# Optimization experiments

Hardware: AMD Instinct MI355X
Metric: run time of the kernel (lower is better)

The kernel has to match this reference:

```python
import jax, jax.numpy as jnp
import numpy as np

EARTH_RADIUS = 6371.0
TAU = 75.0
EPS = 1e-9


def setup_inputs() -> dict:
    key = jax.random.key(0)
    k1, k2, k3 = jax.random.split(key, 3)
    B, C = 512, 32768
    pred_logits = jax.random.normal(k1, (B, C), dtype=jnp.float32)
    # lat in [-90, 90], lon in [-180, 180]
    u_true = jax.random.uniform(k2, (B, 2), dtype=jnp.float32)
    latlon = u_true * jnp.array([180.0, 360.0], jnp.float32) - jnp.array([90.0, 180.0], jnp.float32)
    u_geo = jax.random.uniform(k3, (C, 2), dtype=jnp.float32)
    geocell_coords = u_geo * jnp.array([180.0, 360.0], jnp.float32) - jnp.array([90.0, 180.0], jnp.float32)
    return {"pred_logits": pred_logits, "latlon": latlon, "geocell_coords": geocell_coords}


def _haversine_matrix(latlon, geocell_coords):
    # latlon: [B,2] degrees, geocell_coords: [C,2] degrees -> [B,C] km
    t = jnp.deg2rad(latlon)          # [B,2]
    g = jnp.deg2rad(geocell_coords)  # [C,2]
    lat1 = t[:, 0:1]                 # [B,1]
    lon1 = t[:, 1:2]
    lat2 = g[None, :, 0]             # [1,C]
    lon2 = g[None, :, 1]
    dlat = lat2 - lat1               # [B,C]
    dlon = lon2 - lon1
    a = jnp.sin(dlat * 0.5) ** 2 + jnp.cos(lat1) * jnp.cos(lat2) * jnp.sin(dlon * 0.5) ** 2
    return 2.0 * EARTH_RADIUS * jnp.arcsin(jnp.sqrt(a))


def reference(pred_logits, latlon, geocell_coords):
    dist = _haversine_matrix(latlon, geocell_coords)          # [B,C]
    target = jnp.exp(-dist / TAU)                              # [B,C]
    target = target / jnp.sum(target, axis=1, keepdims=True)
    pred_probs = jax.nn.softmax(pred_logits, axis=1)
    loss = jnp.mean(jnp.sum(-target * jnp.log(pred_probs + EPS), axis=1))
    return loss
```

## Files before the change

kernel.cpp:

```cpp
#include <hip/hip_runtime.h>
#include <math.h>

#define PI_F 3.14159265358979323846f

__global__ void geo_precompute(const float* __restrict__ geo,
                               float4* __restrict__ tab, int C,
                               float* __restrict__ out) {
    int c = blockIdx.x * blockDim.x + threadIdx.x;
    if (c == 0) out[0] = 0.0f;
    if (c >= C) return;
    float lat = geo[2 * c + 0] * (PI_F / 180.0f);
    float lon = geo[2 * c + 1] * (PI_F / 180.0f);
    float sla, cla, slo, clo;
    __sincosf(lat, &sla, &cla);
    __sincosf(lon, &slo, &clo);
    tab[c] = make_float4(cla * clo, cla * slo, sla, 0.0f);
}

__device__ __forceinline__ void pair_accum(float l, float4 g,
                                           float v1x, float v1y, float v1z,
                                           float& Z, float& S0, float& S1) {
    float dot = fmaf(g.x, v1x, fmaf(g.y, v1y, g.z * v1z));
    float a = fmaf(dot, -0.5f, 0.5f);
    a = fmaxf(a, 0.0f);
    float x = __builtin_amdgcn_sqrtf(a);
    float omx = fmaxf(1.0f - x, 0.0f);
    float s = __builtin_amdgcn_sqrtf(omx);
    float p = fmaf(fmaf(fmaf(-0.0187293f, x, 0.0742610f), x, -0.2121144f),
                   x, 1.5707288f);
    float wexp = fmaf(169.8933333f, s * p, -266.867824f);
    float w = __expf(wexp);
    float ez = __expf(l);
    Z += ez;
    S0 += w;
    S1 = fmaf(w, l, S1);
}

__global__ __launch_bounds__(1024) void loss_kernel(
    const float* __restrict__ logits, const float* __restrict__ latlon,
    const float4* __restrict__ tab, float* __restrict__ out,
    int C, float inv_B) {
    const int b = blockIdx.x;
    const int tid = threadIdx.x;

    float lat = latlon[2 * b + 0] * (PI_F / 180.0f);
    float lon = latlon[2 * b + 1] * (PI_F / 180.0f);
    float sla, cla, slo, clo;
    __sincosf(lat, &sla, &cla);
    __sincosf(lon, &slo, &clo);
    const float v1x = cla * clo, v1y = cla * slo, v1z = sla;

    const float4* lp = (const float4*)(logits + (size_t)b * C);
    const int n4 = C >> 2;

    float Z = 0.0f, S0 = 0.0f, S1 = 0.0f;

    for (int i = tid; i < n4; i += 1024) {
        float4 l4 = lp[i];
        const float4* t = tab + 4 * i;
        float4 t0 = t[0], t1 = t[1], t2 = t[2], t3 = t[3];
        pair_accum(l4.x, t0, v1x, v1y, v1z, Z, S0, S1);
        pair_accum(l4.y, t1, v1x, v1y, v1z, Z, S0, S1);
        pair_accum(l4.z, t2, v1x, v1y, v1z, Z, S0, S1);
        pair_accum(l4.w, t3, v1x, v1y, v1z, Z, S0, S1);
    }

    for (int off = 32; off > 0; off >>= 1) {
        Z += __shfl_down(Z, off);
        S0 += __shfl_down(S0, off);
        S1 += __shfl_down(S1, off);
    }
    __shared__ float sZ[16], sS0[16], sS1[16];
    const int wave = tid >> 6, lane = tid & 63;
    if (lane == 0) { sZ[wave] = Z; sS0[wave] = S0; sS1[wave] = S1; }
    __syncthreads();
    if (tid < 64) {
        Z = (tid < 16) ? sZ[tid] : 0.0f;
        S0 = (tid < 16) ? sS0[tid] : 0.0f;
        S1 = (tid < 16) ? sS1[tid] : 0.0f;
        for (int off = 8; off > 0; off >>= 1) {
            Z += __shfl_down(Z, off);
            S0 += __shfl_down(S0, off);
            S1 += __shfl_down(S1, off);
        }
        if (tid == 0) {
            float loss_b = logf(Z) - S1 / S0;
            atomicAdd(out, loss_b * inv_B);
        }
    }
}

extern "C" void kernel_launch(void* const* d_in, const int* in_sizes, int n_in,
                              void* d_out, int out_size, void* d_ws, size_t ws_size,
                              hipStream_t stream) {
    const float* logits = (const float*)d_in[0];
    const float* latlon = (const float*)d_in[1];
    const float* geo    = (const float*)d_in[2];
    float* out = (float*)d_out;

    const int B = in_sizes[1] / 2;
    const int C = in_sizes[2] / 2;
    float4* tab = (float4*)d_ws;

    geo_precompute<<<(C + 255) / 256, 256, 0, stream>>>(geo, tab, C, out);
    loss_kernel<<<B, 1024, 0, stream>>>(logits, latlon, tab, out, C, 1.0f / (float)B);
}
```

Baseline: 111.4 us.

## Tile loss over row blocks and column chunks with deterministic two-stage reduction

Replaces the one-block-per-row kernel with a 2D grid where each block handles 8 rows over a 4096-column chunk. Each geocell table entry is then loaded once and reused across 8 rows. The haversine-to-exp chain is replaced by a single cubic polynomial in the dot product times sqrt(1-dot), fed to exp2, which drops a sqrt and some ALU work per pair. Per-chunk partials go to workspace and a single-block finalize kernel reduces them instead of using atomics. The cost is an extra launch, more registers per thread, and a new polynomial approximation whose accuracy differs from the old one.

```diff
diff --git a/kernel.cpp b/kernel.cpp
--- a/kernel.cpp
+++ b/kernel.cpp
@@ -2,91 +2,140 @@
 #include <math.h>
 
 #define PI_F 3.14159265358979323846f
+#define LOG2E_F 1.4426950408889634f
 
-__global__ void geo_precompute(const float* __restrict__ geo,
-                               float4* __restrict__ tab, int C,
-                               float* __restrict__ out) {
-    int c = blockIdx.x * blockDim.x + threadIdx.x;
-    if (c == 0) out[0] = 0.0f;
-    if (c >= C) return;
-    float lat = geo[2 * c + 0] * (PI_F / 180.0f);
-    float lon = geo[2 * c + 1] * (PI_F / 180.0f);
-    float sla, cla, slo, clo;
-    __sincosf(lat, &sla, &cla);
-    __sincosf(lon, &slo, &clo);
-    tab[c] = make_float4(cla * clo, cla * slo, sla, 0.0f);
+#define A0c -192.49617f
+#define A1c  25.995080f
+#define A2c  -9.1008444f
+#define A3c   2.2953158f
+
+constexpr int CHUNK = 4096;
+constexpr int ROWS  = 8;
+constexpr int TPB   = 512;
+
+__global__ void precompute(const float* __restrict__ geo,
+                           const float* __restrict__ latlon,
+                           float4* __restrict__ tab, float4* __restrict__ rowtab,
+                           int C, int B) {
+    int i = blockIdx.x * blockDim.x + threadIdx.x;
+    if (i < C) {
+        float lat = geo[2 * i + 0] * (PI_F / 180.0f);
+        float lon = geo[2 * i + 1] * (PI_F / 180.0f);
+        float sla, cla, slo, clo;
+        __sincosf(lat, &sla, &cla);
+        __sincosf(lon, &slo, &clo);
+        tab[i] = make_float4(cla * clo, cla * slo, sla, 0.0f);
+    }
+    if (i < B) {
+        float lat = latlon[2 * i + 0] * (PI_F / 180.0f);
+        float lon = latlon[2 * i + 1] * (PI_F / 180.0f);
+        float sla, cla, slo, clo;
+        __sincosf(lat, &sla, &cla);
+        __sincosf(lon, &slo, &clo);
+        rowtab[i] = make_float4(cla * clo, cla * slo, sla, 0.0f);
+    }
 }
 
 __device__ __forceinline__ void pair_accum(float l, float4 g,
-                                           float v1x, float v1y, float v1z,
+                                           float vx, float vy, float vz,
                                            float& Z, float& S0, float& S1) {
-    float dot = fmaf(g.x, v1x, fmaf(g.y, v1y, g.z * v1z));
-    float a = fmaf(dot, -0.5f, 0.5f);
-    a = fmaxf(a, 0.0f);
-    float x = __builtin_amdgcn_sqrtf(a);
-    float omx = fmaxf(1.0f - x, 0.0f);
-    float s = __builtin_amdgcn_sqrtf(omx);
-    float p = fmaf(fmaf(fmaf(-0.0187293f, x, 0.0742610f), x, -0.2121144f),
-                   x, 1.5707288f);
-    float wexp = fmaf(169.8933333f, s * p, -266.867824f);
-    float w = __expf(wexp);
-    float ez = __expf(l);
-    Z += ez;
+    float dot = fmaf(g.x, vx, fmaf(g.y, vy, g.z * vz));
+    float s = __builtin_amdgcn_sqrtf(fmaxf(fmaf(dot, -1.0f, 1.0f), 0.0f));
+    float P = fmaf(fmaf(fmaf(A3c, dot, A2c), dot, A1c), dot, A0c);
+    float w = exp2f(s * P);
+    float el = exp2f(l * LOG2E_F);
+    Z += el;
     S0 += w;
     S1 = fmaf(w, l, S1);
 }
 
-__global__ __launch_bounds__(1024) void loss_kernel(
-    const float* __restrict__ logits, const float* __restrict__ latlon,
-    const float4* __restrict__ tab, float* __restrict__ out,
-    int C, float inv_B) {
-    const int b = blockIdx.x;
-    const int tid = threadIdx.x;
+__global__ __launch_bounds__(TPB, 4) void loss2d(
+    const float* __restrict__ logits, const float4* __restrict__ tab,
+    const float4* __restrict__ rowtab, float4* __restrict__ part, int C, int B) {
+    const int chunk = blockIdx.x;
+    const int rowbase = blockIdx.y * ROWS;
+    const int t = threadIdx.x;
 
-    float lat = latlon[2 * b + 0] * (PI_F / 180.0f);
-    float lon = latlon[2 * b + 1] * (PI_F / 180.0f);
-    float sla, cla, slo, clo;
-    __sincosf(lat, &sla, &cla);
-    __sincosf(lon, &slo, &clo);
-    const float v1x = cla * clo, v1y = cla * slo, v1z = sla;
+    float vx[ROWS], vy[ROWS], vz[ROWS];
+#pragma unroll
+    for (int r = 0; r < ROWS; r++) {
+        float4 v = rowtab[rowbase + r];
+        vx[r] = v.x; vy[r] = v.y; vz[r] = v.z;
+    }
+    float Z[ROWS], S0[ROWS], S1[ROWS];
+#pragma unroll
+    for (int r = 0; r < ROWS; r++) { Z[r] = 0.0f; S0[r] = 0.0f; S1[r] = 0.0f; }
 
-    const float4* lp = (const float4*)(logits + (size_t)b * C);
-    const int n4 = C >> 2;
-
-    float Z = 0.0f, S0 = 0.0f, S1 = 0.0f;
-
-    for (int i = tid; i < n4; i += 1024) {
-        float4 l4 = lp[i];
-        const float4* t = tab + 4 * i;
-        float4 t0 = t[0], t1 = t[1], t2 = t[2], t3 = t[3];
-        pair_accum(l4.x, t0, v1x, v1y, v1z, Z, S0, S1);
-        pair_accum(l4.y, t1, v1x, v1y, v1z, Z, S0, S1);
-        pair_accum(l4.z, t2, v1x, v1y, v1z, Z, S0, S1);
-        pair_accum(l4.w, t3, v1x, v1y, v1z, Z, S0, S1);
+    const int c4base = (chunk * CHUNK) >> 2;
+#pragma unroll
+    for (int it = 0; it < CHUNK / (TPB * 4); it++) {
+        const int c4 = c4base + it * TPB + t;
+        const int c = c4 << 2;
+        float4 g0 = tab[c + 0], g1 = tab[c + 1], g2 = tab[c + 2], g3 = tab[c + 3];
+#pragma unroll
+        for (int r = 0; r < ROWS; r++) {
+            float4 l4 = ((const float4*)(logits + (size_t)(rowbase + r) * C))[c4];
+            pair_accum(l4.x, g0, vx[r], vy[r], vz[r], Z[r], S0[r], S1[r]);
+            pair_accum(l4.y, g1, vx[r], vy[r], vz[r], Z[r], S0[r], S1[r]);
+            pair_accum(l4.z, g2, vx[r], vy[r], vz[r], Z[r], S0[r], S1[r]);
+            pair_accum(l4.w, g3, vx[r], vy[r], vz[r], Z[r], S0[r], S1[r]);
+        }
     }
 
-    for (int off = 32; off > 0; off >>= 1) {
-        Z += __shfl_down(Z, off);
-        S0 += __shfl_down(S0, off);
-        S1 += __shfl_down(S1, off);
+#pragma unroll
+    for (int r = 0; r < ROWS; r++) {
+#pragma unroll
+        for (int off = 32; off > 0; off >>= 1) {
+            Z[r] += __shfl_down(Z[r], off);
+            S0[r] += __shfl_down(S0[r], off);
+            S1[r] += __shfl_down(S1[r], off);
+        }
     }
-    __shared__ float sZ[16], sS0[16], sS1[16];
-    const int wave = tid >> 6, lane = tid & 63;
-    if (lane == 0) { sZ[wave] = Z; sS0[wave] = S0; sS1[wave] = S1; }
+    __shared__ float red[TPB / 64][3 * ROWS];
+    const int wave = t >> 6, lane = t & 63;
+    if (lane == 0) {
+#pragma unroll
+        for (int r = 0; r < ROWS; r++) {
+            red[wave][3 * r + 0] = Z[r];
+            red[wave][3 * r + 1] = S0[r];
+            red[wave][3 * r + 2] = S1[r];
+        }
+    }
     __syncthreads();
-    if (tid < 64) {
-        Z = (tid < 16) ? sZ[tid] : 0.0f;
-        S0 = (tid < 16) ? sS0[tid] : 0.0f;
-        S1 = (tid < 16) ? sS1[tid] : 0.0f;
-        for (int off = 8; off > 0; off >>= 1) {
-            Z += __shfl_down(Z, off);
-            S0 += __shfl_down(S0, off);
-            S1 += __shfl_down(S1, off);
+    if (t < 3 * ROWS) {
+        float s = 0.0f;
+#pragma unroll
+        for (int w = 0; w < TPB / 64; w++) s += red[w][t];
+        red[0][t] = s;
+    }
+    __syncthreads();
+    if (t < ROWS) {
+        part[(size_t)chunk * B + rowbase + t] =
+            make_float4(red[0][3 * t + 0], red[0][3 * t + 1], red[0][3 * t + 2], 0.0f);
+    }
+}
+
+__global__ __launch_bounds__(512) void finalize(const float4* __restrict__ part,
+                                                float* __restrict__ out,
+                                                int B, int nchunk, float inv_B) {
+    float total = 0.0f;
+    for (int r = threadIdx.x; r < B; r += blockDim.x) {
+        float Z = 0.0f, S0 = 0.0f, S1 = 0.0f;
+        for (int ch = 0; ch < nchunk; ch++) {
+            float4 p = part[(size_t)ch * B + r];
+            Z += p.x; S0 += p.y; S1 += p.z;
         }
-        if (tid == 0) {
-            float loss_b = logf(Z) - S1 / S0;
-            atomicAdd(out, loss_b * inv_B);
-        }
+        total += logf(Z) - S1 / S0;
+    }
+    for (int off = 32; off > 0; off >>= 1) total += __shfl_down(total, off);
+    __shared__ float s[8];
+    const int wave = threadIdx.x >> 6;
+    if ((threadIdx.x & 63) == 0) s[wave] = total;
+    __syncthreads();
+    if (threadIdx.x == 0) {
+        float tot = 0.0f;
+        for (int w = 0; w < (int)(blockDim.x >> 6); w++) tot += s[w];
+        out[0] = tot * inv_B;
     }
 }
 
@@ -100,8 +149,15 @@
 
     const int B = in_sizes[1] / 2;
     const int C = in_sizes[2] / 2;
-    float4* tab = (float4*)d_ws;
+    const int nchunk = C / CHUNK;
 
-    geo_precompute<<<(C + 255) / 256, 256, 0, stream>>>(geo, tab, C, out);
-    loss_kernel<<<B, 1024, 0, stream>>>(logits, latlon, tab, out, C, 1.0f / (float)B);
+    float4* tab    = (float4*)d_ws;
+    float4* rowtab = tab + C;
+    float4* part   = rowtab + B;
+
+    int mx = (C > B) ? C : B;
+    precompute<<<(mx + 255) / 256, 256, 0, stream>>>(geo, latlon, tab, rowtab, C, B);
+    dim3 grid(nchunk, B / ROWS);
+    loss2d<<<grid, TPB, 0, stream>>>(logits, tab, rowtab, part, C, B);
+    finalize<<<1, 512, 0, stream>>>(part, out, B, nchunk, 1.0f / (float)B);
 }
```

Result: faster. 107.1 us (-3.9%).
